# Optimization experiments

Hardware: AMD Instinct MI355X
Metric: run time of the kernel (lower is better)

## Reference

```python
import jax, jax.numpy as jnp
import numpy as np

DT = 0.001  # fixed dt in SimplifiedSSM.forward
LN_EPS = 1e-5


def _layernorm(x, g, b):
    m = jnp.mean(x, axis=-1, keepdims=True)
    v = jnp.mean(jnp.square(x - m), axis=-1, keepdims=True)
    return (x - m) * jax.lax.rsqrt(v + LN_EPS) * g + b


def setup_inputs() -> dict:
    key = jax.random.key(0)
    ks = jax.random.split(key, 12)
    Bn, C, H, W = 8, 1024, 32, 32
    depth, S = 4, 128
    d = C
    inp = {
        "x": jax.random.normal(ks[0], (Bn, C, H, W), dtype=jnp.float32),
        # SSM params, stacked over depth. A scaled by 0.1 for numerical stability
        # of the length-1024 recurrence (same math, tamer eigenvalues).
        "A": 0.1 * jax.random.normal(ks[1], (depth, S, S), dtype=jnp.float32),
        "Bp": jax.random.normal(ks[2], (depth, S, d), dtype=jnp.float32),
        "Cp": jax.random.normal(ks[3], (depth, d, S), dtype=jnp.float32),
        "Dp": jax.random.normal(ks[4], (depth, d), dtype=jnp.float32),
        # Linear layers (PyTorch convention: y = x @ W.T + b)
        "Wi": jax.random.normal(ks[5], (depth, d, d), dtype=jnp.float32) / np.sqrt(d),
        "bi": jax.random.normal(ks[6], (depth, d), dtype=jnp.float32) * 0.01,
        "Wo": jax.random.normal(ks[7], (depth, d, d), dtype=jnp.float32) / np.sqrt(d),
        "bo": jax.random.normal(ks[8], (depth, d), dtype=jnp.float32) * 0.01,
        # LayerNorm affine params
        "gamma": jnp.ones((depth, d), dtype=jnp.float32),
        "beta": jnp.zeros((depth, d), dtype=jnp.float32),
    }
    return inp


def reference(x, A, Bp, Cp, Dp, Wi, bi, Wo, bo, gamma, beta):
    Bn, C, H, W = x.shape
    depth, S, _ = A.shape
    # b c h w -> b (h w) c
    seq = x.reshape(Bn, C, H * W).transpose(0, 2, 1)
    eye = jnp.eye(S, dtype=x.dtype)
    for i in range(depth):
        n = _layernorm(seq, gamma[i], beta[i])
        u = n @ Wi[i].T + bi[i]                       # (B, L, d)
        A_bar = eye + DT * A[i]                       # (S, S)
        ub = jnp.einsum('bld,sd->lbs', u, DT * Bp[i]) # (L, B, S)

        def step(h, ub_t):
            h = h @ A_bar.T + ub_t
            return h, h

        h0 = jnp.zeros((Bn, S), dtype=x.dtype)
        _, hs = jax.lax.scan(step, h0, ub)            # hs: (L, B, S)
        y = jnp.einsum('lbs,ds->bld', hs, Cp[i]) + u * Dp[i]
        seq = seq + y @ Wo[i].T + bo[i]
    return seq.transpose(0, 2, 1).reshape(Bn, C, H, W)
```

## Files before the change

kernel.cpp:

```cpp
#include <hip/hip_runtime.h>
#include <stdint.h>

#define DT_STEP 0.001f
#define LN_EPS  1e-5f
#define Bn      8
#define Lseq    1024
#define Dm      1024
#define Sn      128
#define DEPTH   4
#define Mrows   (Bn * Lseq)
#define Qc      32
#define NCHUNK  (Lseq / Qc)
#define NPOW    33

typedef short bf16x8 __attribute__((ext_vector_type(8)));
typedef float f32x4  __attribute__((ext_vector_type(4)));

__device__ __forceinline__ unsigned short f2bf(float f) {
    unsigned int u = __float_as_uint(f);
    u += 0x7fffu + ((u >> 16) & 1u);
    return (unsigned short)(u >> 16);
}

#define GLOAD_LDS16(gp, lp)                                                \
    __builtin_amdgcn_global_load_lds(                                      \
        (const __attribute__((address_space(1))) unsigned int*)(gp),       \
        (__attribute__((address_space(3))) unsigned int*)(lp), 16, 0, 0)

__global__ __launch_bounds__(256) void prep_conv(const float* __restrict__ Wo,
                                                 const float* __restrict__ Dp,
                                                 const float* __restrict__ Bp,
                                                 unsigned short* __restrict__ Woh,
                                                 unsigned short* __restrict__ Wo2h,
                                                 unsigned short* __restrict__ Bph) {
    int z = blockIdx.y;
    int bx = blockIdx.x;
    if (bx < 1024) {
        int i = (bx * 256 + threadIdx.x) * 4;
        const float* S = Wo + (size_t)z * Dm * Dm;
        float4 v = *(const float4*)(S + i);
        int c = i & (Dm - 1);
        float4 d = *(const float4*)(Dp + (size_t)z * Dm + c);
        ushort4 o1, o2;
        o1.x = f2bf(v.x); o1.y = f2bf(v.y); o1.z = f2bf(v.z); o1.w = f2bf(v.w);
        o2.x = f2bf(v.x * d.x); o2.y = f2bf(v.y * d.y);
        o2.z = f2bf(v.z * d.z); o2.w = f2bf(v.w * d.w);
        *(ushort4*)(Woh  + (size_t)z * Dm * Dm + i) = o1;
        *(ushort4*)(Wo2h + (size_t)z * Dm * Dm + i) = o2;
    } else {
        int i = ((bx - 1024) * 256 + threadIdx.x) * 4;
        float4 v = *(const float4*)(Bp + (size_t)z * Sn * Dm + i);
        ushort4 o;
        o.x = f2bf(v.x); o.y = f2bf(v.y); o.z = f2bf(v.z); o.w = f2bf(v.w);
        *(ushort4*)(Bph + (size_t)z * Sn * Dm + i) = o;
    }
}

__global__ __launch_bounds__(256) void transpose_f2bf(const float* __restrict__ src,
                                                      unsigned short* __restrict__ dst,
                                                      int R, int C) {
    __shared__ float t[32][33];
    int z = blockIdx.z;
    const float* S = src + (size_t)z * R * C;
    unsigned short* D = dst + (size_t)z * R * C;
    int r0 = blockIdx.y * 32, c0 = blockIdx.x * 32;
    int tx = threadIdx.x & 31, ty = threadIdx.x >> 5;
    for (int rr = ty; rr < 32; rr += 8)
        t[rr][tx] = S[(size_t)(r0 + rr) * C + c0 + tx];
    __syncthreads();
    for (int rr = ty; rr < 32; rr += 8)
        D[(size_t)(c0 + rr) * R + r0 + tx] = f2bf(t[tx][rr]);
}

__global__ __launch_bounds__(256) void c2dt_boeff(const float* __restrict__ Bp,
                                                  const float* __restrict__ bi,
                                                  const float* __restrict__ Wo,
                                                  const float* __restrict__ Dp,
                                                  const float* __restrict__ bo,
                                                  float* __restrict__ c2dt,
                                                  float* __restrict__ boeff) {
    int z = blockIdx.x, j = blockIdx.y;
    int tid = threadIdx.x;
    float acc;
    if (j < Sn) {
        const float* br = Bp + ((size_t)z * Sn + j) * Dm;
        const float* bb = bi + (size_t)z * Dm;
        float4 v = *(const float4*)(br + tid * 4);
        float4 w = *(const float4*)(bb + tid * 4);
        acc = v.x * w.x + v.y * w.y + v.z * w.z + v.w * w.w;
    } else {
        int c = j - Sn;
        const float* wr = Wo + ((size_t)z * Dm + c) * Dm;
        const float* dp = Dp + (size_t)z * Dm;
        const float* bb = bi + (size_t)z * Dm;
        float4 w = *(const float4*)(wr + tid * 4);
        float4 d = *(const float4*)(dp + tid * 4);
        float4 b = *(const float4*)(bb + tid * 4);
        acc = w.x * d.x * b.x + w.y * d.y * b.y + w.z * d.z * b.z + w.w * d.w * b.w;
    }
#pragma unroll
    for (int off = 32; off > 0; off >>= 1) acc += __shfl_down(acc, off, 64);
    __shared__ float red[4];
    if ((tid & 63) == 0) red[tid >> 6] = acc;
    __syncthreads();
    if (tid == 0) {
        float tot = red[0] + red[1] + red[2] + red[3];
        if (j < Sn) c2dt[z * Sn + j] = DT_STEP * tot;
        else        boeff[(size_t)z * Dm + (j - Sn)] = bo[(size_t)z * Dm + (j - Sn)] + tot;
    }
}

__global__ __launch_bounds__(1024) void transpose_bll(const float* __restrict__ src,
                                                      float* __restrict__ dst) {
    __shared__ float tile[32][33];
    int b  = blockIdx.z;
    int i0 = blockIdx.y * 32, j0 = blockIdx.x * 32;
    int tx = threadIdx.x, ty = threadIdx.y;
    const float* S = src + (size_t)b * Dm * Lseq;
    float*       D = dst + (size_t)b * Dm * Lseq;
    tile[ty][tx] = S[(size_t)(j0 + ty) * 1024 + i0 + tx];
    __syncthreads();
    D[(size_t)(i0 + ty) * 1024 + j0 + tx] = tile[tx][ty];
}

__global__ __launch_bounds__(256) void ln_kernel(const float* __restrict__ x,
                                                 unsigned short* __restrict__ outp,
                                                 const float* __restrict__ g,
                                                 const float* __restrict__ bta) {
    int row = blockIdx.x;
    int tid = threadIdx.x;
    const float* xr = x + (size_t)row * Dm;
    float4 v = *(const float4*)(xr + tid * 4);
    float s  = v.x + v.y + v.z + v.w;
    float ss = v.x * v.x + v.y * v.y + v.z * v.z + v.w * v.w;
#pragma unroll
    for (int off = 32; off > 0; off >>= 1) {
        s  += __shfl_down(s, off, 64);
        ss += __shfl_down(ss, off, 64);
    }
    __shared__ float red[8];
    __shared__ float mv[2];
    int wave = tid >> 6, lane = tid & 63;
    if (lane == 0) { red[wave] = s; red[4 + wave] = ss; }
    __syncthreads();
    if (tid == 0) {
        float st  = red[0] + red[1] + red[2] + red[3];
        float sst = red[4] + red[5] + red[6] + red[7];
        float mean = st / (float)Dm;
        float var  = sst / (float)Dm - mean * mean;
        mv[0] = mean;
        mv[1] = rsqrtf(var + LN_EPS);
    }
    __syncthreads();
    float mean = mv[0], rstd = mv[1];
    int c = tid * 4;
    float4 gv = *(const float4*)(g + c);
    float4 bv = *(const float4*)(bta + c);
    ushort4 o;
    o.x = f2bf((v.x - mean) * rstd * gv.x + bv.x);
    o.y = f2bf((v.y - mean) * rstd * gv.y + bv.y);
    o.z = f2bf((v.z - mean) * rstd * gv.z + bv.z);
    o.w = f2bf((v.w - mean) * rstd * gv.w + bv.w);
    *(ushort4*)(outp + (size_t)row * Dm + c) = o;
}

__global__ __launch_bounds__(512) void gemm_ub(
    const unsigned short* __restrict__ A,
    const unsigned short* __restrict__ B,
    float* __restrict__ ub,
    const float* __restrict__ c2dtL) {
    __shared__ __align__(16) unsigned short As[256 * 8];
    __shared__ __align__(16) unsigned short Bs[1024 * 8];
    int row0 = blockIdx.x * 32;
    int tid  = threadIdx.x;
    int wave = tid >> 6, lane = tid & 63;
    int wn = wave * 16;
    int lr = lane & 15, lq = lane >> 4;

    int rowA = tid >> 3;
    int kclA = (tid & 7) ^ ((tid >> 3) & 7);
    int rowS[2], kclS[2], slotOff[2];
#pragma unroll
    for (int q = 0; q < 2; q++) {
        int s = tid + q * 512;
        rowS[q] = s >> 3;
        kclS[q] = (s & 7) ^ ((s >> 3) & 7);
        slotOff[q] = s * 8;
    }
    int aoff[2][2], boff[2];
#pragma unroll
    for (int i = 0; i < 2; i++)
#pragma unroll
        for (int h = 0; h < 2; h++) {
            int ra = i * 16 + lr;
            aoff[i][h] = (ra * 8 + ((lq + 4 * h) ^ (ra & 7))) * 8;
        }
#pragma unroll
    for (int h = 0; h < 2; h++) {
        int rn = wn + lr;
        boff[h] = (rn * 8 + ((lq + 4 * h) ^ (rn & 7))) * 8;
    }

    f32x4 acc[2];
#pragma unroll
    for (int i = 0; i < 2; i++) acc[i] = (f32x4){0.f, 0.f, 0.f, 0.f};

    for (int k0 = 0; k0 < Dm; k0 += 64) {
        const unsigned short* Abr = A + (size_t)row0 * Dm + k0;
        const unsigned short* Bbr = B + k0;
        __syncthreads();
        if (tid < 256)
            GLOAD_LDS16(Abr + (size_t)rowA * Dm + kclA * 8, &As[tid * 8]);
#pragma unroll
        for (int q = 0; q < 2; q++)
            GLOAD_LDS16(Bbr + (size_t)rowS[q] * Dm + kclS[q] * 8, &Bs[slotOff[q]]);
        __syncthreads();
#pragma unroll
        for (int h = 0; h < 2; h++) {
            bf16x8 af[2], bfr;
#pragma unroll
            for (int i = 0; i < 2; i++) af[i] = *(const bf16x8*)&As[aoff[i][h]];
            bfr = *(const bf16x8*)&Bs[boff[h]];
#pragma unroll
            for (int i = 0; i < 2; i++)
                acc[i] = __builtin_amdgcn_mfma_f32_16x16x32_bf16(af[i], bfr,
                                                                 acc[i], 0, 0, 0);
        }
    }
#pragma unroll
    for (int i = 0; i < 2; i++)
#pragma unroll
        for (int r = 0; r < 4; r++) {
            int row = row0 + i * 16 + lq * 4 + r;
            int col = wn + lr;
            ub[(size_t)row * Sn + col] = acc[i][r] + c2dtL[col];
        }
}

__global__ __launch_bounds__(512) void gemm_bk64(
    const unsigned short* __restrict__ A1, int sA1,
    const unsigned short* __restrict__ A2, int sA2, int KA1,
    const unsigned short* __restrict__ B1, int sB1,
    const unsigned short* __restrict__ B2, int sB2,
    float* __restrict__ Cf, unsigned short* __restrict__ Ch,
    const float* __restrict__ bias1, const float* __restrict__ bias2,
    int ny, int N, int K, float scale, int mode,
    long batchA, long batchB, long batchC) {
    __shared__ __align__(16) unsigned short As[1024 * 8];
    __shared__ __align__(16) unsigned short Bs[1024 * 8];
    int flat = blockIdx.x;
    int rb = flat % ny, cb = flat / ny;
    int row0 = rb * 128, col0 = cb * 128;
    int z = blockIdx.y;
    int tid  = threadIdx.x;
    int wave = tid >> 6, lane = tid & 63;
    int wm = (wave & 1) * 64, wn = (wave >> 1) * 32;
    int lr = lane & 15, lq = lane >> 4;

    int rowS[2], kclS[2], slotOff[2];
#pragma unroll
    for (int q = 0; q < 2; q++) {
        int s = tid + q * 512;
        rowS[q] = s >> 3;
        kclS[q] = (s & 7) ^ ((s >> 3) & 7);
        slotOff[q] = s * 8;
    }
    int aoff[4][2], boff[2][2];
#pragma unroll
    for (int i = 0; i < 4; i++)
#pragma unroll
        for (int h = 0; h < 2; h++) {
            int ra = wm + i * 16 + lr;
            aoff[i][h] = (ra * 8 + ((lq + 4 * h) ^ (ra & 7))) * 8;
        }
#pragma unroll
    for (int j = 0; j < 2; j++)
#pragma unroll
        for (int h = 0; h < 2; h++) {
            int rn = wn + j * 16 + lr;
            boff[j][h] = (rn * 8 + ((lq + 4 * h) ^ (rn & 7))) * 8;
        }

    const unsigned short* A1b = A1 + (size_t)z * batchA;
    const unsigned short* BfixBlk = nullptr;
    int sBfix = sB1;
    if (mode == 2) {
        BfixBlk = B1 + (size_t)z * batchB + (size_t)col0 * sB1;
        sBfix = sB1;
    }

    f32x4 acc[4][2];
#pragma unroll
    for (int i = 0; i < 4; i++)
#pragma unroll
        for (int j = 0; j < 2; j++) acc[i][j] = (f32x4){0.f, 0.f, 0.f, 0.f};

    for (int k0 = 0; k0 < K; k0 += 64) {
        const unsigned short *Ab, *Bb;
        int sa, sb, ko;
        if (mode == 1) {
            if (k0 < KA1) { Ab = A1; sa = sA1; Bb = B1 + (size_t)col0 * sB1; sb = sB1; ko = k0; }
            else          { Ab = A2; sa = sA2; Bb = B2 + (size_t)col0 * sB2; sb = sB2; ko = k0 - KA1; }
        } else {
            Ab = A1b; sa = sA1; Bb = BfixBlk; sb = sBfix; ko = k0;
        }
        const unsigned short* Abr = Ab + (size_t)row0 * sa + ko;
        const unsigned short* Bbr = Bb + ko;
        __syncthreads();
#pragma unroll
        for (int q = 0; q < 2; q++) {
            GLOAD_LDS16(Abr + (size_t)rowS[q] * sa + kclS[q] * 8, &As[slotOff[q]]);
            GLOAD_LDS16(Bbr + (size_t)rowS[q] * sb + kclS[q] * 8, &Bs[slotOff[q]]);
        }
        __syncthreads();
#pragma unroll
        for (int h = 0; h < 2; h++) {
            bf16x8 af[4], bfr[2];
#pragma unroll
            for (int i = 0; i < 4; i++) af[i]  = *(const bf16x8*)&As[aoff[i][h]];
#pragma unroll
            for (int j = 0; j < 2; j++) bfr[j] = *(const bf16x8*)&Bs[boff[j][h]];
#pragma unroll
            for (int i = 0; i < 4; i++)
#pragma unroll
                for (int j = 0; j < 2; j++)
                    acc[i][j] = __builtin_amdgcn_mfma_f32_16x16x32_bf16(af[i], bfr[j],
                                                                       acc[i][j], 0, 0, 0);
        }
    }
#pragma unroll
    for (int i = 0; i < 4; i++) {
#pragma unroll
        for (int j = 0; j < 2; j++) {
#pragma unroll
            for (int r = 0; r < 4; r++) {
                int row = row0 + wm + i * 16 + lq * 4 + r;
                int col = col0 + wn + j * 16 + lr;
                float v = acc[i][j][r];
                if (mode == 1) {
                    size_t idx = (size_t)row * N + col;
                    Cf[idx] = Cf[idx] + v + bias1[col];
                } else {
                    Ch[(size_t)z * batchC + (size_t)row * N + col] = f2bf(v * scale);
                }
            }
        }
    }
}

__global__ __launch_bounds__(128) void pow_init(const float* __restrict__ Amat,
                                                float* __restrict__ Pow) {
    int i = blockIdx.x;
    int s = blockIdx.y;
    int k = threadIdx.x;
    float eye = (s == k) ? 1.f : 0.f;
    size_t base = (size_t)i * NPOW * (Sn * Sn);
    Pow[base + (size_t)s * Sn + k] = eye;
    Pow[base + (size_t)(Sn * Sn) + (size_t)s * Sn + k] =
        eye + DT_STEP * Amat[(size_t)i * Sn * Sn + (size_t)s * Sn + k];
}

__global__ __launch_bounds__(256) void pow_mul(float* __restrict__ Pow, int m, int kmax) {
    int job = blockIdx.z;
    int i  = job / kmax;
    int kk = job % kmax + 1;
    const float* Pa = Pow + ((size_t)i * NPOW + m) * (Sn * Sn);
    const float* Pb = Pow + ((size_t)i * NPOW + kk) * (Sn * Sn);
    float*       Pc = Pow + ((size_t)i * NPOW + m + kk) * (Sn * Sn);
    int r0 = blockIdx.y * 64, c0 = blockIdx.x * 32;
    __shared__ float Asl[64 * 129];
    __shared__ float Bsl[128 * 32];
    int tx = threadIdx.x, ty = threadIdx.y;
    int tid = ty * 16 + tx;
    for (int idx = tid; idx < 64 * 128; idx += 256) {
        int r = idx >> 7, cc = idx & 127;
        Asl[r * 129 + cc] = Pa[(size_t)(r0 + r) * 128 + cc];
    }
    for (int idx = tid; idx < 128 * 32; idx += 256) {
        int r = idx >> 5, cc = idx & 31;
        Bsl[r * 32 + cc] = Pb[(size_t)r * 128 + c0 + cc];
    }
    __syncthreads();
    float acc[4][2] = {{0.f,0.f},{0.f,0.f},{0.f,0.f},{0.f,0.f}};
    for (int k = 0; k < 128; k++) {
        float b0 = Bsl[k * 32 + tx * 2];
        float b1 = Bsl[k * 32 + tx * 2 + 1];
#pragma unroll
        for (int r = 0; r < 4; r++) {
            float a = Asl[(ty * 4 + r) * 129 + k];
            acc[r][0] += a * b0;
            acc[r][1] += a * b1;
        }
    }
#pragma unroll
    for (int r = 0; r < 4; r++) {
        Pc[(size_t)(r0 + ty * 4 + r) * 128 + c0 + tx * 2]     = acc[r][0];
        Pc[(size_t)(r0 + ty * 4 + r) * 128 + c0 + tx * 2 + 1] = acc[r][1];
    }
}

__global__ __launch_bounds__(128) void local_scan(const float* __restrict__ ub,
                                                  float* __restrict__ hs,
                                                  const float* __restrict__ Abar) {
    int b = blockIdx.x / NCHUNK;
    int c = blockIdx.x % NCHUNK;
    int s = threadIdx.x;
    float arow[Sn];
#pragma unroll
    for (int k = 0; k < Sn; k += 4) {
        float4 v = *(const float4*)(Abar + (size_t)s * Sn + k);
        arow[k] = v.x; arow[k + 1] = v.y; arow[k + 2] = v.z; arow[k + 3] = v.w;
    }
    __shared__ __align__(16) float hsh[Sn];
    hsh[s] = 0.f;
    __syncthreads();
    size_t base = (size_t)(b * Lseq + c * Qc) * Sn + s;
    float ut = ub[base];
    for (int t = 0; t < Qc; t++) {
        float utn = (t + 1 < Qc) ? ub[base + (size_t)(t + 1) * Sn] : 0.f;
        float a0 = 0.f, a1 = 0.f, a2 = 0.f, a3 = 0.f;
#pragma unroll
        for (int k = 0; k < Sn; k += 16) {
            float4 h0 = *(const float4*)&hsh[k];
            float4 h1 = *(const float4*)&hsh[k + 4];
            float4 h2 = *(const float4*)&hsh[k + 8];
            float4 h3 = *(const float4*)&hsh[k + 12];
            a0 += arow[k + 0] * h0.x + arow[k + 1] * h0.y + arow[k + 2] * h0.z + arow[k + 3] * h0.w;
            a1 += arow[k + 4] * h1.x + arow[k + 5] * h1.y + arow[k + 6] * h1.z + arow[k + 7] * h1.w;
            a2 += arow[k + 8] * h2.x + arow[k + 9] * h2.y + arow[k + 10] * h2.z + arow[k + 11] * h2.w;
            a3 += arow[k + 12] * h3.x + arow[k + 13] * h3.y + arow[k + 14] * h3.z + arow[k + 15] * h3.w;
        }
        float hv = ut + (a0 + a1) + (a2 + a3);
        hs[base + (size_t)t * Sn] = hv;
        __syncthreads();
        hsh[s] = hv;
        __syncthreads();
        ut = utn;
    }
}

__global__ __launch_bounds__(128) void carry_scan(const float* __restrict__ hs,
                                                  const float* __restrict__ AQ,
                                                  float* __restrict__ carry) {
    int b = blockIdx.x;
    int s = threadIdx.x;
    float le[NCHUNK];
#pragma unroll
    for (int c = 0; c < NCHUNK; c++)
        le[c] = hs[(size_t)(b * Lseq + c * Qc + Qc - 1) * Sn + s];
    float arow[Sn];
#pragma unroll
    for (int k = 0; k < Sn; k += 4) {
        float4 v = *(const float4*)(AQ + (size_t)s * Sn + k);
        arow[k] = v.x; arow[k + 1] = v.y; arow[k + 2] = v.z; arow[k + 3] = v.w;
    }
    __shared__ __align__(16) float csh[Sn];
    csh[s] = 0.f;
    __syncthreads();
    for (int c = 0; c < NCHUNK; c++) {
        carry[((size_t)b * NCHUNK + c) * Sn + s] = csh[s];
        float a0 = 0.f, a1 = 0.f, a2 = 0.f, a3 = 0.f;
#pragma unroll
        for (int k = 0; k < Sn; k += 16) {
            float4 h0 = *(const float4*)&csh[k];
            float4 h1 = *(const float4*)&csh[k + 4];
            float4 h2 = *(const float4*)&csh[k + 8];
            float4 h3 = *(const float4*)&csh[k + 12];
            a0 += arow[k + 0] * h0.x + arow[k + 1] * h0.y + arow[k + 2] * h0.z + arow[k + 3] * h0.w;
            a1 += arow[k + 4] * h1.x + arow[k + 5] * h1.y + arow[k + 6] * h1.z + arow[k + 7] * h1.w;
            a2 += arow[k + 8] * h2.x + arow[k + 9] * h2.y + arow[k + 10] * h2.z + arow[k + 11] * h2.w;
            a3 += arow[k + 12] * h3.x + arow[k + 13] * h3.y + arow[k + 14] * h3.z + arow[k + 15] * h3.w;
        }
        float cv = le[c] + (a0 + a1) + (a2 + a3);
        __syncthreads();
        csh[s] = cv;
        __syncthreads();
    }
}

__global__ __launch_bounds__(256) void fixup_scan(const float* __restrict__ hs,
                                                  unsigned short* __restrict__ hs_bf,
                                                  const float* __restrict__ PowLayer,
                                                  const float* __restrict__ carry) {
    int t  = blockIdx.x;
    int c4 = blockIdx.y;
    const float* P = PowLayer + (size_t)(t + 1) * (Sn * Sn);
    __shared__ float Pl[Sn * 65];
    __shared__ float cl[4][Bn * Sn];
    int tid = threadIdx.x;
#pragma unroll
    for (int cc = 0; cc < 4; cc++)
        for (int idx = tid; idx < Bn * Sn; idx += 256)
            cl[cc][idx] = carry[((size_t)(idx >> 7) * NCHUNK + (c4 * 4 + cc)) * Sn + (idx & 127)];
    int s = tid & 127, bh = tid >> 7;
    float acc[4][4];
#pragma unroll
    for (int cc = 0; cc < 4; cc++)
#pragma unroll
        for (int j = 0; j < 4; j++) acc[cc][j] = 0.f;
    for (int kh = 0; kh < 2; kh++) {
        __syncthreads();
        for (int idx = tid; idx < Sn * 64; idx += 256) {
            int r = idx >> 6, kk = idx & 63;
            Pl[r * 65 + kk] = P[(size_t)r * Sn + kh * 64 + kk];
        }
        __syncthreads();
        for (int kk = 0; kk < 64; kk++) {
            float pw = Pl[s * 65 + kk];
            int kg = kh * 64 + kk;
#pragma unroll
            for (int cc = 0; cc < 4; cc++)
#pragma unroll
                for (int j = 0; j < 4; j++)
                    acc[cc][j] += pw * cl[cc][(bh * 4 + j) * Sn + kg];
        }
    }
#pragma unroll
    for (int cc = 0; cc < 4; cc++) {
        int c = c4 * 4 + cc;
#pragma unroll
        for (int j = 0; j < 4; j++) {
            int bb = bh * 4 + j;
            size_t rowi = (size_t)(bb * Lseq + c * Qc + t) * Sn + s;
            hs_bf[rowi] = f2bf(hs[rowi] + acc[cc][j]);
        }
    }
}

extern "C" void kernel_launch(void* const* d_in, const int* in_sizes, int n_in,
                              void* d_out, int out_size, void* d_ws, size_t ws_size,
                              hipStream_t stream) {
    const float* x     = (const float*)d_in[0];
    const float* Am    = (const float*)d_in[1];
    const float* Bp    = (const float*)d_in[2];
    const float* Cp    = (const float*)d_in[3];
    const float* Dp    = (const float*)d_in[4];
    const float* Wi    = (const float*)d_in[5];
    const float* bi    = (const float*)d_in[6];
    const float* Wo    = (const float*)d_in[7];
    const float* bo    = (const float*)d_in[8];
    const float* gamma = (const float*)d_in[9];
    const float* beta  = (const float*)d_in[10];
    float* out = (float*)d_out;
    (void)in_sizes; (void)n_in; (void)out_size; (void)ws_size;

    char* ws = (char*)d_ws;
    float*          seq   = (float*)(ws + (size_t)0);
    unsigned short* nbuf  = (unsigned short*)(ws + (size_t)33554432);
    unsigned short* WiTh  = (unsigned short*)(ws + (size_t)33554432);
    unsigned short* Woh   = (unsigned short*)(ws + (size_t)41943040);
    unsigned short* W4h   = (unsigned short*)(ws + (size_t)50331648);
    float*          boeff = (float*)(ws + (size_t)58720256);
    float*          ub    = (float*)(ws + (size_t)67108864);
    float*          hs    = (float*)(ws + (size_t)71303168);
    unsigned short* hs_bf = (unsigned short*)(ws + (size_t)75497472);
    float*          Pow   = (float*)(ws + (size_t)77594624);
    float*          carry = (float*)(ws + (size_t)86245376);
    unsigned short* Wo2h  = (unsigned short*)(ws + (size_t)94765056);
    unsigned short* Bph   = (unsigned short*)(ws + (size_t)103153664);
    unsigned short* CpTh  = (unsigned short*)(ws + (size_t)104202240);
    unsigned short* M2h   = (unsigned short*)(ws + (size_t)105250816);
    unsigned short* W3h   = (unsigned short*)(ws + (size_t)106299392);
    float*          c2dt  = (float*)(ws + (size_t)107347968);

    const long WW = (long)Dm * Dm;
    const long SW = (long)Sn * Dm;

    hipLaunchKernelGGL(prep_conv, dim3(1024 + 128, DEPTH), dim3(256), 0, stream,
                       Wo, Dp, Bp, Woh, Wo2h, Bph);
    hipLaunchKernelGGL(transpose_f2bf, dim3(32, 32, DEPTH), dim3(256), 0, stream,
                       Wi, WiTh, Dm, Dm);
    hipLaunchKernelGGL(transpose_f2bf, dim3(4, 32, DEPTH), dim3(256), 0, stream,
                       Cp, CpTh, Dm, Sn);
    hipLaunchKernelGGL(c2dt_boeff, dim3(DEPTH, Sn + Dm), dim3(256), 0, stream,
                       Bp, bi, Wo, Dp, bo, c2dt, boeff);

    hipLaunchKernelGGL(gemm_bk64, dim3(8, DEPTH), dim3(512), 0, stream,
                       Bph, Dm, (const unsigned short*)nullptr, 0, 0,
                       WiTh, Dm, (const unsigned short*)nullptr, 0,
                       (float*)nullptr, M2h, (const float*)nullptr, (const float*)nullptr,
                       1, Dm, Dm, DT_STEP, 2, SW, WW, SW);
    hipLaunchKernelGGL(gemm_bk64, dim3(8, DEPTH), dim3(512), 0, stream,
                       Woh, Dm, (const unsigned short*)nullptr, 0, 0,
                       CpTh, Dm, (const unsigned short*)nullptr, 0,
                       (float*)nullptr, W3h, (const float*)nullptr, (const float*)nullptr,
                       8, Sn, Dm, 1.f, 2, WW, SW, SW);
    hipLaunchKernelGGL(gemm_bk64, dim3(8 * 8, DEPTH), dim3(512), 0, stream,
                       Wo2h, Dm, (const unsigned short*)nullptr, 0, 0,
                       WiTh, Dm, (const unsigned short*)nullptr, 0,
                       (float*)nullptr, W4h, (const float*)nullptr, (const float*)nullptr,
                       8, Dm, Dm, 1.f, 2, WW, WW, WW);

    hipLaunchKernelGGL(transpose_bll, dim3(32, 32, Bn), dim3(32, 32), 0, stream, x, seq);

    hipLaunchKernelGGL(pow_init, dim3(DEPTH, Sn), dim3(Sn), 0, stream, Am, Pow);
    for (int m = 1; m < Qc; m <<= 1) {
        hipLaunchKernelGGL(pow_mul, dim3(4, 2, DEPTH * m), dim3(16, 16), 0, stream,
                           Pow, m, m);
    }

    for (int i = 0; i < DEPTH; i++) {
        const unsigned short* M2_i = M2h + (size_t)i * SW;
        const unsigned short* W3_i = W3h + (size_t)i * SW;
        const unsigned short* W4_i = W4h + (size_t)i * WW;
        const float* PowL = Pow + (size_t)i * NPOW * (Sn * Sn);

        hipLaunchKernelGGL(ln_kernel, dim3(Mrows), dim3(256), 0, stream,
                           seq, nbuf, gamma + i * Dm, beta + i * Dm);
        hipLaunchKernelGGL(gemm_ub, dim3(Mrows / 32), dim3(512), 0, stream,
                           nbuf, M2_i, ub, c2dt + i * Sn);
        hipLaunchKernelGGL(local_scan, dim3(Bn * NCHUNK), dim3(Sn), 0, stream,
                           ub, hs, PowL + (size_t)1 * Sn * Sn);
        hipLaunchKernelGGL(carry_scan, dim3(Bn), dim3(Sn), 0, stream,
                           hs, PowL + (size_t)Qc * Sn * Sn, carry);
        hipLaunchKernelGGL(fixup_scan, dim3(Qc, NCHUNK / 4), dim3(256), 0, stream,
                           hs, hs_bf, PowL, carry);
        hipLaunchKernelGGL(gemm_bk64, dim3(8 * 64, 1), dim3(512), 0, stream,
                           hs_bf, Sn, nbuf, Dm, Sn,
                           W3_i, Sn, W4_i, Dm,
                           seq, (unsigned short*)nullptr, boeff + i * Dm, (const float*)nullptr,
                           64, Dm, Dm + Sn, 1.f, 1, 0, 0, 0);
    }

    hipLaunchKernelGGL(transpose_bll, dim3(32, 32, Bn), dim3(32, 32), 0, stream, seq, out);
}
```

Before: 764.4 us.

## Overlap local chunk scan with W4 GEMM in a single heterogeneous kernel

Splits the fused output GEMM (hs·W3 + n·W4) into two parts. The large n·W4 part no longer depends on the scan, so it runs in the same launch as the local chunk scan: the first 256 blocks do the scan, and the remaining 1024 blocks do a 128x64-tile GEMM that accumulates into seq. The small hs·W3 GEMM runs after the fixup. The scan now uses 512 threads, splitting the 128-wide matvec four ways with a shared-memory reduction, which cuts register pressure but adds synchronisation per step. It also uses narrower 64-column GEMM tiles and reads and writes seq twice per layer.

```diff
diff --git a/kernel.cpp b/kernel.cpp
--- a/kernel.cpp
+++ b/kernel.cpp
@@ -237,14 +237,153 @@
         }
 }
 
+__device__ __forceinline__ void gemm64_body(
+    int flat, unsigned short* As, unsigned short* Bs,
+    const unsigned short* __restrict__ A, const unsigned short* __restrict__ B,
+    float* __restrict__ C, const float* __restrict__ bias, int K) {
+    int rb = flat & 63, cb = flat >> 6;
+    int row0 = rb * 128, col0 = cb * 64;
+    int tid  = threadIdx.x;
+    int wave = tid >> 6, lane = tid & 63;
+    int wm = (wave & 1) * 64, wn = (wave >> 1) * 16;
+    int lr = lane & 15, lq = lane >> 4;
+
+    int rowS[2], kclS[2], slotOff[2];
+#pragma unroll
+    for (int q = 0; q < 2; q++) {
+        int s = tid + q * 512;
+        rowS[q] = s >> 3;
+        kclS[q] = (s & 7) ^ ((s >> 3) & 7);
+        slotOff[q] = s * 8;
+    }
+    int rowB = tid >> 3;
+    int kclB = (tid & 7) ^ ((tid >> 3) & 7);
+
+    int aoff[4][2], boff[2];
+#pragma unroll
+    for (int i = 0; i < 4; i++)
+#pragma unroll
+        for (int h = 0; h < 2; h++) {
+            int ra = wm + i * 16 + lr;
+            aoff[i][h] = (ra * 8 + ((lq + 4 * h) ^ (ra & 7))) * 8;
+        }
+#pragma unroll
+    for (int h = 0; h < 2; h++) {
+        int rn = wn + lr;
+        boff[h] = (rn * 8 + ((lq + 4 * h) ^ (rn & 7))) * 8;
+    }
+
+    f32x4 acc[4];
+#pragma unroll
+    for (int i = 0; i < 4; i++) acc[i] = (f32x4){0.f, 0.f, 0.f, 0.f};
+
+    for (int k0 = 0; k0 < K; k0 += 64) {
+        const unsigned short* Abr = A + (size_t)row0 * K + k0;
+        const unsigned short* Bbr = B + (size_t)col0 * K + k0;
+        __syncthreads();
+#pragma unroll
+        for (int q = 0; q < 2; q++)
+            GLOAD_LDS16(Abr + (size_t)rowS[q] * K + kclS[q] * 8, &As[slotOff[q]]);
+        GLOAD_LDS16(Bbr + (size_t)rowB * K + kclB * 8, &Bs[tid * 8]);
+        __syncthreads();
+#pragma unroll
+        for (int h = 0; h < 2; h++) {
+            bf16x8 af[4], bf;
+#pragma unroll
+            for (int i = 0; i < 4; i++) af[i] = *(const bf16x8*)&As[aoff[i][h]];
+            bf = *(const bf16x8*)&Bs[boff[h]];
+#pragma unroll
+            for (int i = 0; i < 4; i++)
+                acc[i] = __builtin_amdgcn_mfma_f32_16x16x32_bf16(af[i], bf,
+                                                                 acc[i], 0, 0, 0);
+        }
+    }
+#pragma unroll
+    for (int i = 0; i < 4; i++)
+#pragma unroll
+        for (int r = 0; r < 4; r++) {
+            int row = row0 + wm + i * 16 + lq * 4 + r;
+            int col = col0 + wn + lr;
+            size_t idx = (size_t)row * Dm + col;
+            float v = acc[i][r];
+            if (bias) v += bias[col];
+            C[idx] = C[idx] + v;
+        }
+}
+
+__global__ __launch_bounds__(512) void gemm_w3k(const unsigned short* __restrict__ hs_bf,
+                                                const unsigned short* __restrict__ W3,
+                                                float* __restrict__ seq) {
+    __shared__ __align__(16) unsigned short As[1024 * 8];
+    __shared__ __align__(16) unsigned short Bs[512 * 8];
+    gemm64_body(blockIdx.x, As, Bs, hs_bf, W3, seq, nullptr, Sn);
+}
+
+__global__ __launch_bounds__(512) void mega_scan_w4(
+    const unsigned short* __restrict__ nbuf,
+    const unsigned short* __restrict__ W4,
+    float* __restrict__ seq,
+    const float* __restrict__ boeff,
+    const float* __restrict__ ub,
+    float* __restrict__ hs,
+    const float* __restrict__ Abar) {
+    __shared__ __align__(16) unsigned short As[1024 * 8];
+    __shared__ __align__(16) unsigned short Bs[512 * 8];
+    __shared__ __align__(16) float hsh[Sn];
+    __shared__ __align__(16) float hp[4][Sn];
+    int tid = threadIdx.x;
+
+    if (blockIdx.x >= 256) {
+        gemm64_body(blockIdx.x - 256, As, Bs, nbuf, W4, seq, boeff, Dm);
+        return;
+    }
+
+    int chunk = blockIdx.x;
+    int b = chunk >> 5;
+    int c = chunk & 31;
+    int s = tid & 127, kq = tid >> 7;
+    float arow[32];
+#pragma unroll
+    for (int j = 0; j < 32; j += 4) {
+        float4 v = *(const float4*)(Abar + (size_t)s * Sn + kq * 32 + j);
+        arow[j] = v.x; arow[j + 1] = v.y; arow[j + 2] = v.z; arow[j + 3] = v.w;
+    }
+    if (tid < 128) hsh[tid] = 0.f;
+    __syncthreads();
+    size_t base = (size_t)(b * Lseq + c * Qc) * Sn + s;
+    float ut = (kq == 0) ? ub[base] : 0.f;
+    const float* hq = &hsh[kq * 32];
+    for (int t = 0; t < Qc; t++) {
+        float utn = (kq == 0 && t + 1 < Qc) ? ub[base + (size_t)(t + 1) * Sn] : 0.f;
+        float a0 = 0.f, a1 = 0.f, a2 = 0.f, a3 = 0.f;
+#pragma unroll
+        for (int j = 0; j < 32; j += 16) {
+            float4 h0 = *(const float4*)&hq[j];
+            float4 h1 = *(const float4*)&hq[j + 4];
+            float4 h2 = *(const float4*)&hq[j + 8];
+            float4 h3 = *(const float4*)&hq[j + 12];
+            a0 += arow[j + 0] * h0.x + arow[j + 1] * h0.y + arow[j + 2] * h0.z + arow[j + 3] * h0.w;
+            a1 += arow[j + 4] * h1.x + arow[j + 5] * h1.y + arow[j + 6] * h1.z + arow[j + 7] * h1.w;
+            a2 += arow[j + 8] * h2.x + arow[j + 9] * h2.y + arow[j + 10] * h2.z + arow[j + 11] * h2.w;
+            a3 += arow[j + 12] * h3.x + arow[j + 13] * h3.y + arow[j + 14] * h3.z + arow[j + 15] * h3.w;
+        }
+        hp[kq][s] = (a0 + a1) + (a2 + a3);
+        __syncthreads();
+        if (kq == 0) {
+            float hv = ut + (hp[0][s] + hp[1][s]) + (hp[2][s] + hp[3][s]);
+            hs[base + (size_t)t * Sn] = hv;
+            hsh[s] = hv;
+        }
+        __syncthreads();
+        ut = utn;
+    }
+}
+
 __global__ __launch_bounds__(512) void gemm_bk64(
     const unsigned short* __restrict__ A1, int sA1,
-    const unsigned short* __restrict__ A2, int sA2, int KA1,
     const unsigned short* __restrict__ B1, int sB1,
-    const unsigned short* __restrict__ B2, int sB2,
-    float* __restrict__ Cf, unsigned short* __restrict__ Ch,
-    const float* __restrict__ bias1, const float* __restrict__ bias2,
-    int ny, int N, int K, float scale, int mode,
+    unsigned short* __restrict__ Ch,
+    int ny, int N, int K, float scale,
     long batchA, long batchB, long batchC) {
     __shared__ __align__(16) unsigned short As[1024 * 8];
     __shared__ __align__(16) unsigned short Bs[1024 * 8];
@@ -281,13 +420,8 @@
             boff[j][h] = (rn * 8 + ((lq + 4 * h) ^ (rn & 7))) * 8;
         }
 
-    const unsigned short* A1b = A1 + (size_t)z * batchA;
-    const unsigned short* BfixBlk = nullptr;
-    int sBfix = sB1;
-    if (mode == 2) {
-        BfixBlk = B1 + (size_t)z * batchB + (size_t)col0 * sB1;
-        sBfix = sB1;
-    }
+    const unsigned short* Ab = A1 + (size_t)z * batchA;
+    const unsigned short* Bb = B1 + (size_t)z * batchB + (size_t)col0 * sB1;
 
     f32x4 acc[4][2];
 #pragma unroll
@@ -296,21 +430,13 @@
         for (int j = 0; j < 2; j++) acc[i][j] = (f32x4){0.f, 0.f, 0.f, 0.f};
 
     for (int k0 = 0; k0 < K; k0 += 64) {
-        const unsigned short *Ab, *Bb;
-        int sa, sb, ko;
-        if (mode == 1) {
-            if (k0 < KA1) { Ab = A1; sa = sA1; Bb = B1 + (size_t)col0 * sB1; sb = sB1; ko = k0; }
-            else          { Ab = A2; sa = sA2; Bb = B2 + (size_t)col0 * sB2; sb = sB2; ko = k0 - KA1; }
-        } else {
-            Ab = A1b; sa = sA1; Bb = BfixBlk; sb = sBfix; ko = k0;
-        }
-        const unsigned short* Abr = Ab + (size_t)row0 * sa + ko;
-        const unsigned short* Bbr = Bb + ko;
+        const unsigned short* Abr = Ab + (size_t)row0 * sA1 + k0;
+        const unsigned short* Bbr = Bb + k0;
         __syncthreads();
 #pragma unroll
         for (int q = 0; q < 2; q++) {
-            GLOAD_LDS16(Abr + (size_t)rowS[q] * sa + kclS[q] * 8, &As[slotOff[q]]);
-            GLOAD_LDS16(Bbr + (size_t)rowS[q] * sb + kclS[q] * 8, &Bs[slotOff[q]]);
+            GLOAD_LDS16(Abr + (size_t)rowS[q] * sA1 + kclS[q] * 8, &As[slotOff[q]]);
+            GLOAD_LDS16(Bbr + (size_t)rowS[q] * sB1 + kclS[q] * 8, &Bs[slotOff[q]]);
         }
         __syncthreads();
 #pragma unroll
@@ -329,23 +455,15 @@
         }
     }
 #pragma unroll
-    for (int i = 0; i < 4; i++) {
-#pragma unroll
-        for (int j = 0; j < 2; j++) {
+    for (int i = 0; i < 4; i++)
+#pragma unroll
+        for (int j = 0; j < 2; j++)
 #pragma unroll
             for (int r = 0; r < 4; r++) {
                 int row = row0 + wm + i * 16 + lq * 4 + r;
                 int col = col0 + wn + j * 16 + lr;
-                float v = acc[i][j][r];
-                if (mode == 1) {
-                    size_t idx = (size_t)row * N + col;
-                    Cf[idx] = Cf[idx] + v + bias1[col];
-                } else {
-                    Ch[(size_t)z * batchC + (size_t)row * N + col] = f2bf(v * scale);
-                }
+                Ch[(size_t)z * batchC + (size_t)row * N + col] = f2bf(acc[i][j][r] * scale);
             }
-        }
-    }
 }
 
 __global__ __launch_bounds__(128) void pow_init(const float* __restrict__ Amat,
@@ -396,46 +514,6 @@
     for (int r = 0; r < 4; r++) {
         Pc[(size_t)(r0 + ty * 4 + r) * 128 + c0 + tx * 2]     = acc[r][0];
         Pc[(size_t)(r0 + ty * 4 + r) * 128 + c0 + tx * 2 + 1] = acc[r][1];
-    }
-}
-
-__global__ __launch_bounds__(128) void local_scan(const float* __restrict__ ub,
-                                                  float* __restrict__ hs,
-                                                  const float* __restrict__ Abar) {
-    int b = blockIdx.x / NCHUNK;
-    int c = blockIdx.x % NCHUNK;
-    int s = threadIdx.x;
-    float arow[Sn];
-#pragma unroll
-    for (int k = 0; k < Sn; k += 4) {
-        float4 v = *(const float4*)(Abar + (size_t)s * Sn + k);
-        arow[k] = v.x; arow[k + 1] = v.y; arow[k + 2] = v.z; arow[k + 3] = v.w;
-    }
-    __shared__ __align__(16) float hsh[Sn];
-    hsh[s] = 0.f;
-    __syncthreads();
-    size_t base = (size_t)(b * Lseq + c * Qc) * Sn + s;
-    float ut = ub[base];
-    for (int t = 0; t < Qc; t++) {
-        float utn = (t + 1 < Qc) ? ub[base + (size_t)(t + 1) * Sn] : 0.f;
-        float a0 = 0.f, a1 = 0.f, a2 = 0.f, a3 = 0.f;
-#pragma unroll
-        for (int k = 0; k < Sn; k += 16) {
-            float4 h0 = *(const float4*)&hsh[k];
-            float4 h1 = *(const float4*)&hsh[k + 4];
-            float4 h2 = *(const float4*)&hsh[k + 8];
-            float4 h3 = *(const float4*)&hsh[k + 12];
-            a0 += arow[k + 0] * h0.x + arow[k + 1] * h0.y + arow[k + 2] * h0.z + arow[k + 3] * h0.w;
-            a1 += arow[k + 4] * h1.x + arow[k + 5] * h1.y + arow[k + 6] * h1.z + arow[k + 7] * h1.w;
-            a2 += arow[k + 8] * h2.x + arow[k + 9] * h2.y + arow[k + 10] * h2.z + arow[k + 11] * h2.w;
-            a3 += arow[k + 12] * h3.x + arow[k + 13] * h3.y + arow[k + 14] * h3.z + arow[k + 15] * h3.w;
-        }
-        float hv = ut + (a0 + a1) + (a2 + a3);
-        hs[base + (size_t)t * Sn] = hv;
-        __syncthreads();
-        hsh[s] = hv;
-        __syncthreads();
-        ut = utn;
     }
 }
 
@@ -576,20 +654,11 @@
                        Bp, bi, Wo, Dp, bo, c2dt, boeff);
 
     hipLaunchKernelGGL(gemm_bk64, dim3(8, DEPTH), dim3(512), 0, stream,
-                       Bph, Dm, (const unsigned short*)nullptr, 0, 0,
-                       WiTh, Dm, (const unsigned short*)nullptr, 0,
-                       (float*)nullptr, M2h, (const float*)nullptr, (const float*)nullptr,
-                       1, Dm, Dm, DT_STEP, 2, SW, WW, SW);
+                       Bph, Dm, WiTh, Dm, M2h, 1, Dm, Dm, DT_STEP, SW, WW, SW);
     hipLaunchKernelGGL(gemm_bk64, dim3(8, DEPTH), dim3(512), 0, stream,
-                       Woh, Dm, (const unsigned short*)nullptr, 0, 0,
-                       CpTh, Dm, (const unsigned short*)nullptr, 0,
-                       (float*)nullptr, W3h, (const float*)nullptr, (const float*)nullptr,
-                       8, Sn, Dm, 1.f, 2, WW, SW, SW);
+                       Woh, Dm, CpTh, Dm, W3h, 8, Sn, Dm, 1.f, WW, SW, SW);
     hipLaunchKernelGGL(gemm_bk64, dim3(8 * 8, DEPTH), dim3(512), 0, stream,
-                       Wo2h, Dm, (const unsigned short*)nullptr, 0, 0,
-                       WiTh, Dm, (const unsigned short*)nullptr, 0,
-                       (float*)nullptr, W4h, (const float*)nullptr, (const float*)nullptr,
-                       8, Dm, Dm, 1.f, 2, WW, WW, WW);
+                       Wo2h, Dm, WiTh, Dm, W4h, 8, Dm, Dm, 1.f, WW, WW, WW);
 
     hipLaunchKernelGGL(transpose_bll, dim3(32, 32, Bn), dim3(32, 32), 0, stream, x, seq);
 
@@ -609,17 +678,15 @@
                            seq, nbuf, gamma + i * Dm, beta + i * Dm);
         hipLaunchKernelGGL(gemm_ub, dim3(Mrows / 32), dim3(512), 0, stream,
                            nbuf, M2_i, ub, c2dt + i * Sn);
-        hipLaunchKernelGGL(local_scan, dim3(Bn * NCHUNK), dim3(Sn), 0, stream,
-                           ub, hs, PowL + (size_t)1 * Sn * Sn);
+        hipLaunchKernelGGL(mega_scan_w4, dim3(256 + 1024), dim3(512), 0, stream,
+                           nbuf, W4_i, seq, boeff + i * Dm,
+                           ub, hs, PowL + (size_t)Sn * Sn);
         hipLaunchKernelGGL(carry_scan, dim3(Bn), dim3(Sn), 0, stream,
                            hs, PowL + (size_t)Qc * Sn * Sn, carry);
         hipLaunchKernelGGL(fixup_scan, dim3(Qc, NCHUNK / 4), dim3(256), 0, stream,
                            hs, hs_bf, PowL, carry);
-        hipLaunchKernelGGL(gemm_bk64, dim3(8 * 64, 1), dim3(512), 0, stream,
-                           hs_bf, Sn, nbuf, Dm, Sn,
-                           W3_i, Sn, W4_i, Dm,
-                           seq, (unsigned short*)nullptr, boeff + i * Dm, (const float*)nullptr,
-                           64, Dm, Dm + Sn, 1.f, 1, 0, 0, 0);
+        hipLaunchKernelGGL(gemm_w3k, dim3(1024), dim3(512), 0, stream,
+                           hs_bf, W3_i, seq);
     }
 
     hipLaunchKernelGGL(transpose_bll, dim3(32, 32, Bn), dim3(32, 32), 0, stream, seq, out);
```

After: 740.4 us. 1.03x faster.
